# Optimization experiments

Measured on AMD Instinct MI355X. Metric: run time of the kernel, lower is better.

Reference implementation:

```python
import jax, jax.numpy as jnp
import numpy as np

B, N, DIN, DOUT, H, DH, DC, NL, L = 8, 256, 64, 64, 8, 8, 64, 32, 2
SCALE = DH ** -0.5  # out_dim-per-head scaling used by both attention variants


def _ln(x, g, b):
    m = jnp.mean(x, -1, keepdims=True)
    v = jnp.mean((x - m) ** 2, -1, keepdims=True)
    return (x - m) * jax.lax.rsqrt(v + 1e-5) * g + b


def _cross_attn(x, ctx, mask_b, wq, wkv, wo, bo):
    # CrossAttentionLayer: standard softmax attention with clamp(-5,5)
    b, n, _ = x.shape
    m = ctx.shape[1]
    q = (x @ wq).reshape(b, n, H, DH).transpose(0, 2, 1, 3)
    k, v = jnp.split(ctx @ wkv, 2, axis=-1)
    k = k.reshape(b, m, H, DH).transpose(0, 2, 1, 3)
    v = v.reshape(b, m, H, DH).transpose(0, 2, 1, 3)
    sim = jnp.einsum('bhid,bhjd->bhij', q, k) * SCALE
    if mask_b is not None:
        sim = jnp.where(mask_b[:, None, None, :], sim, -jnp.finfo(sim.dtype).max)
    sim = jnp.clip(sim, -5.0, 5.0)
    attn = jax.nn.softmax(sim, axis=-1)
    out = jnp.einsum('bhij,bhjd->bhid', attn, v)
    out = out.transpose(0, 2, 1, 3).reshape(b, n, H * DH)
    return out @ wo + bo


def _mha_edge(p, e, k_RW, mask, wq, wk, we, wv):
    # GraphiT MultiHeadAttentionLayer with edge features + k_RW attention PE
    Q = (p @ wq).reshape(B, N, H, DH)
    K = (p @ wk).reshape(B, N, H, DH) * SCALE
    V = (p @ wv).reshape(B, N, H, DH).transpose(0, 2, 1, 3)  # [B,H,N,d]
    E = (e @ we).reshape(B, N, N, H, DH)
    scores = jnp.einsum('bihk,bjhk,bijhk->bhij', Q, K, E)
    scores = jnp.exp(scores - jnp.max(scores, axis=(-2, -1), keepdims=True))
    scores = scores * mask[:, None, :, None] * mask[:, None, None, :]
    scores = scores * k_RW
    denom = jnp.clip(jnp.sum(scores, -1, keepdims=True), 1e-6, None)
    out = jnp.einsum('bhij,bhjd->bhid', scores, V) / denom
    return out.transpose(0, 2, 1, 3).reshape(B, N, H * DH)


def setup_inputs() -> dict:
    key = jax.random.key(0)
    ks = jax.random.split(key, 32)
    rn = lambda k, s: jax.random.normal(k, s, dtype=jnp.float32)
    inp = {
        'h': rn(ks[0], (B, N, DIN)),
        'p': rn(ks[1], (B, N, DIN)),
        'e': rn(ks[2], (B, N, N, DIN)),
        'k_RW': jax.random.uniform(ks[3], (B, 1, N, N), dtype=jnp.float32),
        'queries': rn(ks[4], (B, NL, DC)),
        'mask': jnp.ones((B, N), dtype=jnp.float32),
        # attention_p (MultiHeadAttentionLayer) weights
        'wq_p': rn(ks[5], (DIN, H * DH)) * 0.05,
        'wk_p': rn(ks[6], (DIN, H * DH)) * 0.05,
        'we_p': rn(ks[7], (DIN, H * DH)) * 0.05,
        'wv_p': rn(ks[8], (DIN, H * DH)) * 0.05,
        'wo_p': rn(ks[9], (DOUT, DOUT)) * 0.05,
        # cross_attention_h (queries attend to nodes)
        'cq_wq': rn(ks[10], (DC, H * DH)) * 0.05,
        'cq_wkv': rn(ks[11], (DIN, 2 * H * DH)) * 0.05,
        'cq_wo': rn(ks[12], (H * DH, DC)) * 0.05,
        'cq_bo': jnp.zeros((DC,), dtype=jnp.float32),
        # L_cross latent self-attention layers (stacked)
        'sa_wq': rn(ks[13], (L, DC, H * DH)) * 0.05,
        'sa_wkv': rn(ks[14], (L, DC, 2 * H * DH)) * 0.05,
        'sa_wo': rn(ks[15], (L, H * DH, DC)) * 0.05,
        'sa_bo': jnp.zeros((L, DC), dtype=jnp.float32),
        # O_queries, norms, FFN
        'oq_w': rn(ks[16], (DC, DC)) * 0.05,
        'ln1_g': jnp.ones((DC,), dtype=jnp.float32),
        'ln1_b': jnp.zeros((DC,), dtype=jnp.float32),
        'ffn_w1': rn(ks[17], (DC, 2 * DC)) * 0.05,
        'ffn_w2': rn(ks[18], (2 * DC, DC)) * 0.05,
        'ln2_g': jnp.ones((DC,), dtype=jnp.float32),
        'ln2_b': jnp.zeros((DC,), dtype=jnp.float32),
    }
    return inp


def reference(h, p, e, k_RW, queries, mask,
              wq_p, wk_p, we_p, wv_p, wo_p,
              cq_wq, cq_wkv, cq_wo, cq_bo,
              sa_wq, sa_wkv, sa_wo, sa_bo,
              oq_w, ln1_g, ln1_b, ffn_w1, ffn_w2, ln2_g, ln2_b):
    # forward_p: update positional encoding via edge-modulated attention
    p_attn = _mha_edge(p, e, k_RW, mask, wq_p, wk_p, we_p, wv_p)
    p_new = p + jnp.tanh(p_attn @ wo_p)  # residual, no dropout (eval)
    # combine node features with updated PE (use_node_pe='sum')
    h_c = h + p_new
    mask_b = mask > 0.5
    # perceiver cross-attention: latents attend to nodes
    q = queries + _cross_attn(queries, h_c, mask_b, cq_wq, cq_wkv, cq_wo, cq_bo)
    # L_cross latent self-attention blocks with residual
    for i in range(L):
        q = q + _cross_attn(q, q, None, sa_wq[i], sa_wkv[i], sa_wo[i], sa_bo[i])
    # O_queries projection + layer norm
    q = _ln(q @ oq_w, ln1_g, ln1_b)
    # feed-forward block on queries
    ff = jax.nn.relu(q @ ffn_w1) @ ffn_w2
    q = _ln(q + ff, ln2_g, ln2_b)
    return q
```

## Files before the change

### kernel.cpp

```cpp
#include <hip/hip_runtime.h>
#include <hip/hip_bf16.h>
#include <math.h>

typedef __bf16 bf16x8 __attribute__((ext_vector_type(8)));
typedef float floatx4 __attribute__((ext_vector_type(4)));

#define ATT_SCALE 0.35355339059327373f

__device__ __forceinline__ __bf16 f2b(float x) { return (__bf16)x; }

__global__ __launch_bounds__(256) void k_proj(const float* __restrict__ p,
                       const float* __restrict__ wq, const float* __restrict__ wk,
                       const float* __restrict__ wv,
                       float* __restrict__ Q, float* __restrict__ Ks,
                       float* __restrict__ V) {
  int blk = blockIdx.x, t = threadIdx.x;
  __shared__ float xr[8][64];
  {
    int rr = t >> 5, cc = (t & 31) * 2;
    float2 pz = *reinterpret_cast<const float2*>(p + blk * 512 + rr * 64 + cc);
    xr[rr][cc] = pz.x; xr[rr][cc + 1] = pz.y;
  }
  __syncthreads();
  if (t < 192) {
    int mat = t >> 6, c = t & 63;
    const float* w = (mat == 0) ? wq : ((mat == 1) ? wk : wv);
    float acc[8] = {0.f, 0.f, 0.f, 0.f, 0.f, 0.f, 0.f, 0.f};
#pragma unroll 8
    for (int k = 0; k < 64; k++) {
      float wv_ = w[k * 64 + c];
#pragma unroll
      for (int r = 0; r < 8; r++) acc[r] += xr[r][k] * wv_;
    }
    float* dst = (mat == 0) ? Q : ((mat == 1) ? Ks : V);
    float sc = (mat == 1) ? ATT_SCALE : 1.f;
#pragma unroll
    for (int r = 0; r < 8; r++) dst[(blk * 8 + r) * 64 + c] = acc[r] * sc;
  }
}

__global__ __launch_bounds__(256) void k_edge(
    const float* __restrict__ e, const float* __restrict__ we,
    const float* __restrict__ krw, const float* __restrict__ mask,
    const float* __restrict__ hin, const float* __restrict__ pin,
    const float* __restrict__ wo, const float* __restrict__ cq_wkv,
    const float* __restrict__ Q, const float* __restrict__ Ks,
    const float* __restrict__ V, float* __restrict__ Kc, float* __restrict__ Vc) {
  int bi = blockIdx.x;
  int b = bi >> 8;
  int t = threadIdx.x;
  int w = t >> 6, l = t & 63;
  int l15 = l & 15, quad = l >> 4, half8 = (l >> 3) & 1, d = l & 7;

  bf16x8 wfrag[4][2];
  for (int nt = 0; nt < 4; nt++)
    for (int kc = 0; kc < 2; kc++)
      for (int jj = 0; jj < 8; jj++)
        wfrag[nt][kc][jj] = f2b(we[(kc * 32 + quad * 8 + jj) * 64 + nt * 16 + l15]);

  float qv[4];
  for (int nt = 0; nt < 4; nt++) qv[nt] = Q[bi * 64 + nt * 16 + l15];
  float mi = mask[bi];

  float aout[4] = {0.f, 0.f, 0.f, 0.f};
  float aden[4] = {0.f, 0.f, 0.f, 0.f};

  for (int mt = 0; mt < 4; mt++) {
    int j0 = w * 64 + mt * 16;
    const float* ep = e + ((long)bi * 256 + j0 + l15) * 64 + quad * 8;
    float4 ea = *reinterpret_cast<const float4*>(ep);
    float4 eb4 = *reinterpret_cast<const float4*>(ep + 4);
    float4 ec = *reinterpret_cast<const float4*>(ep + 32);
    float4 ed4 = *reinterpret_cast<const float4*>(ep + 36);
    bf16x8 a0, a1;
    a0[0] = f2b(ea.x); a0[1] = f2b(ea.y); a0[2] = f2b(ea.z); a0[3] = f2b(ea.w);
    a0[4] = f2b(eb4.x); a0[5] = f2b(eb4.y); a0[6] = f2b(eb4.z); a0[7] = f2b(eb4.w);
    a1[0] = f2b(ec.x); a1[1] = f2b(ec.y); a1[2] = f2b(ec.z); a1[3] = f2b(ec.w);
    a1[4] = f2b(ed4.x); a1[5] = f2b(ed4.y); a1[6] = f2b(ed4.z); a1[7] = f2b(ed4.w);

    int jr0 = j0 + quad * 4;
    float krw_r[4], mj_r[4];
    for (int r = 0; r < 4; r++) {
      krw_r[r] = krw[(long)bi * 256 + jr0 + r];
      mj_r[r] = mask[b * 256 + jr0 + r];
    }
    for (int nt = 0; nt < 4; nt++) {
      floatx4 acc = {0.f, 0.f, 0.f, 0.f};
      acc = __builtin_amdgcn_mfma_f32_16x16x32_bf16(a0, wfrag[nt][0], acc, 0, 0, 0);
      acc = __builtin_amdgcn_mfma_f32_16x16x32_bf16(a1, wfrag[nt][1], acc, 0, 0, 0);
      int hk = nt * 16 + l15;
      int hbase = hk & 56;
      for (int r = 0; r < 4; r++) {
        int jr = jr0 + r;
        float s = acc[r] * qv[nt] * Ks[(b * 256 + jr) * 64 + hk];
        s += __shfl_xor(s, 1);
        s += __shfl_xor(s, 2);
        s += __shfl_xor(s, 4);
        float wg = __expf(s) * krw_r[r] * mj_r[r];
        aden[nt] += wg;
        aout[nt] += wg * V[(b * 256 + jr) * 64 + hbase + d];
      }
    }
  }
  for (int nt = 0; nt < 4; nt++) {
    float o = aout[nt], dn = aden[nt];
    o += __shfl_xor(o, 16); o += __shfl_xor(o, 32);
    dn += __shfl_xor(dn, 16); dn += __shfl_xor(dn, 32);
    aout[nt] = o; aden[nt] = dn;
  }

  __shared__ float red[4][64];
  __shared__ float redden[4][8];
  __shared__ float pav[64];
  __shared__ float hcl[64];
  if (l < 16) {
    for (int nt = 0; nt < 4; nt++) {
      int head = nt * 2 + half8;
      red[w][head * 8 + d] = aout[nt];
      if (d == 0) redden[w][head] = aden[nt];
    }
  }
  __syncthreads();
  if (t < 64) {
    int head = t >> 3;
    float num = red[0][t] + red[1][t] + red[2][t] + red[3][t];
    float den = redden[0][head] + redden[1][head] + redden[2][head] + redden[3][head];
    num *= mi;
    den = fmaxf(den * mi, 1e-6f);
    pav[t] = num / den;
  }
  __syncthreads();
  if (t < 64) {
    float a = 0.f;
    for (int c = 0; c < 64; c++) a += pav[c] * wo[c * 64 + t];
    hcl[t] = hin[bi * 64 + t] + pin[bi * 64 + t] + tanhf(a);
  }
  __syncthreads();
  if (t < 128) {
    float a = 0.f;
    for (int c = 0; c < 64; c++) a += hcl[c] * cq_wkv[c * 128 + t];
    if (t < 64) Kc[bi * 64 + t] = a;
    else        Vc[bi * 64 + t - 64] = a;
  }
}

template <int NR, int NC, int ST>
__device__ __forceinline__ void stage_w(const float* __restrict__ g,
                                        __bf16* wls, int t) {
  constexpr int PER = (NR * NC) >> 10;
  int i0 = t * PER;
  int k = i0 / NC, c0 = i0 % NC;
  const float* src = g + k * NC + c0;
  __bf16* dst = wls + k * ST + c0;
#pragma unroll
  for (int m = 0; m < PER; m += 4) {
    float4 v = *reinterpret_cast<const float4*>(src + m);
    dst[m] = f2b(v.x); dst[m + 1] = f2b(v.y);
    dst[m + 2] = f2b(v.z); dst[m + 3] = f2b(v.w);
  }
}

__global__ __launch_bounds__(1024) void k_tail(
    const float* __restrict__ quer, const float* __restrict__ Kc,
    const float* __restrict__ Vc, const float* __restrict__ mask,
    const float* __restrict__ cq_wq, const float* __restrict__ cq_wo,
    const float* __restrict__ cq_bo,
    const float* __restrict__ sa_wq, const float* __restrict__ sa_wkv,
    const float* __restrict__ sa_wo, const float* __restrict__ sa_bo,
    const float* __restrict__ oq_w, const float* __restrict__ g1,
    const float* __restrict__ b1, const float* __restrict__ w1,
    const float* __restrict__ w2, const float* __restrict__ g2,
    const float* __restrict__ b2v, float* __restrict__ out) {
  int b = blockIdx.x;
  int t = threadIdx.x;

  __shared__ float sq[32 * 68];
  __shared__ float sx[32 * 68];
  __shared__ float pool[6400];
  __shared__ float smask[256];
  __shared__ __bf16 wls[8448];

  float* soc = pool + 4160;
  __bf16* kq = reinterpret_cast<__bf16*>(pool);
  __bf16* vq = kq + 4096;

  const int rr6 = t >> 6, c6 = t & 63;
  const int r2 = t >> 5, h = (t >> 2) & 7, s = t & 3;

  {
    float2 qz = *reinterpret_cast<const float2*>(quer + b * 2048 + (t >> 5) * 64 + (t & 31) * 2);
    sq[(t >> 5) * 68 + (t & 31) * 2] = qz.x;
    sq[(t >> 5) * 68 + (t & 31) * 2 + 1] = qz.y;
    if (t < 256) smask[t] = mask[b * 256 + t];
    stage_w<64, 64, 66>(cq_wq, wls, t);
  }
  __syncthreads();

  {
    float a0 = 0.f, a1 = 0.f;
#pragma unroll 8
    for (int k = 0; k < 64; k++) {
      float wv = (float)wls[k * 66 + c6];
      a0 += sq[rr6 * 68 + k] * wv;
      a1 += sq[(rr6 + 16) * 68 + k] * wv;
    }
    sx[rr6 * 68 + c6] = a0;
    sx[(rr6 + 16) * 68 + c6] = a1;
  }
  __syncthreads();

  float num[8] = {0.f, 0.f, 0.f, 0.f, 0.f, 0.f, 0.f, 0.f};
  float den = 0.f;
  {
    float qv8[8];
#pragma unroll
    for (int dd = 0; dd < 8; dd++) qv8[dd] = sx[r2 * 68 + h * 8 + dd];
    for (int qtr = 0; qtr < 4; qtr++) {
      {
        int half = t >> 9, idx = t & 511;
        int jl = idx >> 3, c0 = (idx & 7) * 8;
        const float* src = (half ? Vc : Kc) + ((long)(b * 256 + qtr * 64 + jl)) * 64 + c0;
        __bf16* dst = (half ? vq : kq) + jl * 64 + c0;
        float4 u = *reinterpret_cast<const float4*>(src);
        float4 v = *reinterpret_cast<const float4*>(src + 4);
        dst[0] = f2b(u.x); dst[1] = f2b(u.y); dst[2] = f2b(u.z); dst[3] = f2b(u.w);
        dst[4] = f2b(v.x); dst[5] = f2b(v.y); dst[6] = f2b(v.z); dst[7] = f2b(v.w);
      }
      if (qtr == 0) stage_w<64, 64, 66>(cq_wo, wls, t);
      __syncthreads();
#pragma unroll
      for (int jj = 0; jj < 16; jj++) {
        int jl = jj * 4 + s;
        bf16x8 kk = *reinterpret_cast<const bf16x8*>(kq + jl * 64 + h * 8);
        float sc = qv8[0] * (float)kk[0] + qv8[1] * (float)kk[1]
                 + qv8[2] * (float)kk[2] + qv8[3] * (float)kk[3]
                 + qv8[4] * (float)kk[4] + qv8[5] * (float)kk[5]
                 + qv8[6] * (float)kk[6] + qv8[7] * (float)kk[7];
        sc *= ATT_SCALE;
        sc = (smask[qtr * 64 + jl] > 0.5f) ? sc : -1e30f;
        sc = fminf(fmaxf(sc, -5.f), 5.f);
        float ex = __expf(sc);
        den += ex;
        bf16x8 vv = *reinterpret_cast<const bf16x8*>(vq + jl * 64 + h * 8);
#pragma unroll
        for (int dd = 0; dd < 8; dd++) num[dd] += ex * (float)vv[dd];
      }
      __syncthreads();
    }
    den += __shfl_xor(den, 1); den += __shfl_xor(den, 2);
#pragma unroll
    for (int dd = 0; dd < 8; dd++) {
      float v = num[dd];
      v += __shfl_xor(v, 1); v += __shfl_xor(v, 2);
      num[dd] = v;
    }
    if (s == 0) {
      float inv = 1.f / den;
#pragma unroll
      for (int dd = 0; dd < 8; dd++) soc[r2 * 68 + h * 8 + dd] = num[dd] * inv;
    }
  }
  __syncthreads();

  {
    float a0 = 0.f, a1 = 0.f;
#pragma unroll 8
    for (int k = 0; k < 64; k++) {
      float wv = (float)wls[k * 66 + c6];
      a0 += soc[rr6 * 68 + k] * wv;
      a1 += soc[(rr6 + 16) * 68 + k] * wv;
    }
    float bb = cq_bo[c6];
    sq[rr6 * 68 + c6] += a0 + bb;
    sq[(rr6 + 16) * 68 + c6] += a1 + bb;
  }
  __syncthreads();

  for (int layer = 0; layer < 2; layer++) {
    const float* wql = sa_wq + layer * 4096;
    const float* wkvl = sa_wkv + layer * 8192;
    const float* wol = sa_wo + layer * 4096;
    const float* bol = sa_bo + layer * 64;

    stage_w<64, 64, 66>(wql, wls, t);
    __syncthreads();
    {
      float a0 = 0.f, a1 = 0.f;
#pragma unroll 8
      for (int k = 0; k < 64; k++) {
        float wv = (float)wls[k * 66 + c6];
        a0 += sq[rr6 * 68 + k] * wv;
        a1 += sq[(rr6 + 16) * 68 + k] * wv;
      }
      sx[rr6 * 68 + c6] = a0;
      sx[(rr6 + 16) * 68 + c6] = a1;
    }
    __syncthreads();
    stage_w<64, 128, 130>(wkvl, wls, t);
    __syncthreads();
    {
      int rrk = t >> 7, ck = t & 127;
      float a0 = 0.f, a1 = 0.f, a2 = 0.f, a3 = 0.f;
#pragma unroll 8
      for (int k = 0; k < 64; k++) {
        float wv = (float)wls[k * 130 + ck];
        a0 += sq[rrk * 68 + k] * wv;
        a1 += sq[(rrk + 8) * 68 + k] * wv;
        a2 += sq[(rrk + 16) * 68 + k] * wv;
        a3 += sq[(rrk + 24) * 68 + k] * wv;
      }
      float* dst = (ck < 64) ? (pool + rrk * 65 + ck) : (pool + 2080 + rrk * 65 + (ck - 64));
      dst[0] = a0; dst[8 * 65] = a1; dst[16 * 65] = a2; dst[24 * 65] = a3;
    }
    __syncthreads();
    {
      stage_w<64, 64, 66>(wol, wls, t);
      float qv8[8];
#pragma unroll
      for (int dd = 0; dd < 8; dd++) qv8[dd] = sx[r2 * 68 + h * 8 + dd];
      float nm[8] = {0.f, 0.f, 0.f, 0.f, 0.f, 0.f, 0.f, 0.f};
      float dn = 0.f;
#pragma unroll
      for (int jj = 0; jj < 8; jj++) {
        int j = jj * 4 + s;
        const float* kp = pool + j * 65 + h * 8;
        float sc = 0.f;
#pragma unroll
        for (int dd = 0; dd < 8; dd++) sc += qv8[dd] * kp[dd];
        sc *= ATT_SCALE;
        sc = fminf(fmaxf(sc, -5.f), 5.f);
        float ex = __expf(sc);
        dn += ex;
        const float* vp = pool + 2080 + j * 65 + h * 8;
#pragma unroll
        for (int dd = 0; dd < 8; dd++) nm[dd] += ex * vp[dd];
      }
      dn += __shfl_xor(dn, 1); dn += __shfl_xor(dn, 2);
#pragma unroll
      for (int dd = 0; dd < 8; dd++) {
        float v = nm[dd];
        v += __shfl_xor(v, 1); v += __shfl_xor(v, 2);
        nm[dd] = v;
      }
      if (s == 0) {
        float inv = 1.f / dn;
#pragma unroll
        for (int dd = 0; dd < 8; dd++) soc[r2 * 68 + h * 8 + dd] = nm[dd] * inv;
      }
    }
    __syncthreads();
    {
      float a0 = 0.f, a1 = 0.f;
#pragma unroll 8
      for (int k = 0; k < 64; k++) {
        float wv = (float)wls[k * 66 + c6];
        a0 += soc[rr6 * 68 + k] * wv;
        a1 += soc[(rr6 + 16) * 68 + k] * wv;
      }
      float bb = bol[c6];
      sq[rr6 * 68 + c6] += a0 + bb;
      sq[(rr6 + 16) * 68 + c6] += a1 + bb;
    }
    __syncthreads();
  }

  stage_w<64, 64, 66>(oq_w, wls, t);
  __syncthreads();
  {
    float a0 = 0.f, a1 = 0.f;
#pragma unroll 8
    for (int k = 0; k < 64; k++) {
      float wv = (float)wls[k * 66 + c6];
      a0 += sq[rr6 * 68 + k] * wv;
      a1 += sq[(rr6 + 16) * 68 + k] * wv;
    }
    sx[rr6 * 68 + c6] = a0;
    sx[(rr6 + 16) * 68 + c6] = a1;
  }
  __syncthreads();
  {
    int wv_ = t >> 6, lc = t & 63;
#pragma unroll
    for (int pass = 0; pass < 2; pass++) {
      int rr = wv_ + pass * 16;
      float x = sx[rr * 68 + lc];
      float m = x;
      for (int off = 1; off < 64; off <<= 1) m += __shfl_xor(m, off);
      m *= (1.f / 64.f);
      float dv = x - m, vv = dv * dv;
      for (int off = 1; off < 64; off <<= 1) vv += __shfl_xor(vv, off);
      vv *= (1.f / 64.f);
      sx[rr * 68 + lc] = dv * rsqrtf(vv + 1e-5f) * g1[lc] + b1[lc];
    }
    stage_w<64, 128, 130>(w1, wls, t);
  }
  __syncthreads();
  {
    int rrk = t >> 7, ck = t & 127;
    float a0 = 0.f, a1 = 0.f, a2 = 0.f, a3 = 0.f;
#pragma unroll 8
    for (int k = 0; k < 64; k++) {
      float wv = (float)wls[k * 130 + ck];
      a0 += sx[rrk * 68 + k] * wv;
      a1 += sx[(rrk + 8) * 68 + k] * wv;
      a2 += sx[(rrk + 16) * 68 + k] * wv;
      a3 += sx[(rrk + 24) * 68 + k] * wv;
    }
    pool[rrk * 128 + ck] = fmaxf(a0, 0.f);
    pool[(rrk + 8) * 128 + ck] = fmaxf(a1, 0.f);
    pool[(rrk + 16) * 128 + ck] = fmaxf(a2, 0.f);
    pool[(rrk + 24) * 128 + ck] = fmaxf(a3, 0.f);
  }
  __syncthreads();
  stage_w<128, 64, 66>(w2, wls, t);
  __syncthreads();
  {
    int wv_ = t >> 6, lc = t & 63;
#pragma unroll
    for (int pass = 0; pass < 2; pass++) {
      int rr = wv_ + pass * 16;
      float ff = 0.f;
#pragma unroll 8
      for (int k = 0; k < 128; k++) ff += pool[rr * 128 + k] * (float)wls[k * 66 + lc];
      float z = sx[rr * 68 + lc] + ff;
      float m2 = z;
      for (int off = 1; off < 64; off <<= 1) m2 += __shfl_xor(m2, off);
      m2 *= (1.f / 64.f);
      float dz = z - m2, v2 = dz * dz;
      for (int off = 1; off < 64; off <<= 1) v2 += __shfl_xor(v2, off);
      v2 *= (1.f / 64.f);
      out[b * 2048 + rr * 64 + lc] = dz * rsqrtf(v2 + 1e-5f) * g2[lc] + b2v[lc];
    }
  }
}

extern "C" void kernel_launch(void* const* d_in, const int* in_sizes, int n_in,
                              void* d_out, int out_size, void* d_ws, size_t ws_size,
                              hipStream_t stream) {
  const float* h_in   = (const float*)d_in[0];
  const float* p_in   = (const float*)d_in[1];
  const float* e_in   = (const float*)d_in[2];
  const float* krw    = (const float*)d_in[3];
  const float* quer   = (const float*)d_in[4];
  const float* mask   = (const float*)d_in[5];
  const float* wq_p   = (const float*)d_in[6];
  const float* wk_p   = (const float*)d_in[7];
  const float* we_p   = (const float*)d_in[8];
  const float* wv_p   = (const float*)d_in[9];
  const float* wo_p   = (const float*)d_in[10];
  const float* cq_wq  = (const float*)d_in[11];
  const float* cq_wkv = (const float*)d_in[12];
  const float* cq_wo  = (const float*)d_in[13];
  const float* cq_bo  = (const float*)d_in[14];
  const float* sa_wq  = (const float*)d_in[15];
  const float* sa_wkv = (const float*)d_in[16];
  const float* sa_wo  = (const float*)d_in[17];
  const float* sa_bo  = (const float*)d_in[18];
  const float* oq_w   = (const float*)d_in[19];
  const float* ln1_g  = (const float*)d_in[20];
  const float* ln1_b  = (const float*)d_in[21];
  const float* ffn_w1 = (const float*)d_in[22];
  const float* ffn_w2 = (const float*)d_in[23];
  const float* ln2_g  = (const float*)d_in[24];
  const float* ln2_b  = (const float*)d_in[25];

  float* ws = (float*)d_ws;
  float* Q  = ws;
  float* Ks = Q + 131072;
  float* V  = Ks + 131072;
  float* Kc = V + 131072;
  float* Vc = Kc + 131072;

  k_proj<<<256, 256, 0, stream>>>(p_in, wq_p, wk_p, wv_p, Q, Ks, V);
  k_edge<<<2048, 256, 0, stream>>>(e_in, we_p, krw, mask, h_in, p_in, wo_p, cq_wkv,
                                   Q, Ks, V, Kc, Vc);
  k_tail<<<8, 1024, 0, stream>>>(quer, Kc, Vc, mask, cq_wq, cq_wo, cq_bo,
                                 sa_wq, sa_wkv, sa_wo, sa_bo, oq_w,
                                 ln1_g, ln1_b, ffn_w1, ffn_w2, ln2_g, ln2_b,
                                 (float*)d_out);
}
```

Baseline: 333.2 us.

## Register-block four query rows per thread in tail attention loops

The tail kernel's cross-attention and latent self-attention loops now have each thread handle four query rows of one head over a 16-way key split, instead of one row over a 4-way split. Each K/V vector loaded from shared memory is reused across four rows, cutting LDS traffic and bf16 conversions. The bf16 K/V staging rows are padded from 64 to 72 elements to reduce bank conflicts, so the shared pool grows. In exchange, register pressure rises in a 1024-thread block, and the reductions need four shuffle stages per value.

Result: slower. 346.1 us (+3.9%).

```diff
diff --git a/kernel.cpp b/kernel.cpp
--- a/kernel.cpp
+++ b/kernel.cpp
@@ -176,16 +176,16 @@
 
   __shared__ float sq[32 * 68];
   __shared__ float sx[32 * 68];
-  __shared__ float pool[6400];
+  __shared__ float pool[6784];
   __shared__ float smask[256];
   __shared__ __bf16 wls[8448];
 
-  float* soc = pool + 4160;
+  float* soc = pool + 4608;
   __bf16* kq = reinterpret_cast<__bf16*>(pool);
-  __bf16* vq = kq + 4096;
+  __bf16* vq = kq + 4608;
 
   const int rr6 = t >> 6, c6 = t & 63;
-  const int r2 = t >> 5, h = (t >> 2) & 7, s = t & 3;
+  const int rg = t >> 7, h8 = (t >> 4) & 7, s16 = t & 15;
 
   {
     float2 qz = *reinterpret_cast<const float2*>(quer + b * 2048 + (t >> 5) * 64 + (t & 31) * 2);
@@ -209,18 +209,26 @@
   }
   __syncthreads();
 
-  float num[8] = {0.f, 0.f, 0.f, 0.f, 0.f, 0.f, 0.f, 0.f};
-  float den = 0.f;
-  {
-    float qv8[8];
-#pragma unroll
-    for (int dd = 0; dd < 8; dd++) qv8[dd] = sx[r2 * 68 + h * 8 + dd];
+  {
+    float qv8[4][8];
+#pragma unroll
+    for (int rr = 0; rr < 4; rr++)
+#pragma unroll
+      for (int dd = 0; dd < 8; dd++)
+        qv8[rr][dd] = sx[(rg * 4 + rr) * 68 + h8 * 8 + dd];
+    float num[4][8];
+    float den[4] = {0.f, 0.f, 0.f, 0.f};
+#pragma unroll
+    for (int rr = 0; rr < 4; rr++)
+#pragma unroll
+      for (int dd = 0; dd < 8; dd++) num[rr][dd] = 0.f;
+
     for (int qtr = 0; qtr < 4; qtr++) {
       {
         int half = t >> 9, idx = t & 511;
         int jl = idx >> 3, c0 = (idx & 7) * 8;
         const float* src = (half ? Vc : Kc) + ((long)(b * 256 + qtr * 64 + jl)) * 64 + c0;
-        __bf16* dst = (half ? vq : kq) + jl * 64 + c0;
+        __bf16* dst = (half ? vq : kq) + jl * 72 + c0;
         float4 u = *reinterpret_cast<const float4*>(src);
         float4 v = *reinterpret_cast<const float4*>(src + 4);
         dst[0] = f2b(u.x); dst[1] = f2b(u.y); dst[2] = f2b(u.z); dst[3] = f2b(u.w);
@@ -229,35 +237,53 @@
       if (qtr == 0) stage_w<64, 64, 66>(cq_wo, wls, t);
       __syncthreads();
 #pragma unroll
-      for (int jj = 0; jj < 16; jj++) {
-        int jl = jj * 4 + s;
-        bf16x8 kk = *reinterpret_cast<const bf16x8*>(kq + jl * 64 + h * 8);
-        float sc = qv8[0] * (float)kk[0] + qv8[1] * (float)kk[1]
-                 + qv8[2] * (float)kk[2] + qv8[3] * (float)kk[3]
-                 + qv8[4] * (float)kk[4] + qv8[5] * (float)kk[5]
-                 + qv8[6] * (float)kk[6] + qv8[7] * (float)kk[7];
-        sc *= ATT_SCALE;
-        sc = (smask[qtr * 64 + jl] > 0.5f) ? sc : -1e30f;
-        sc = fminf(fmaxf(sc, -5.f), 5.f);
-        float ex = __expf(sc);
-        den += ex;
-        bf16x8 vv = *reinterpret_cast<const bf16x8*>(vq + jl * 64 + h * 8);
-#pragma unroll
-        for (int dd = 0; dd < 8; dd++) num[dd] += ex * (float)vv[dd];
+      for (int jj = 0; jj < 4; jj++) {
+        int jl = jj * 16 + s16;
+        bf16x8 kk = *reinterpret_cast<const bf16x8*>(kq + jl * 72 + h8 * 8);
+        bf16x8 vv = *reinterpret_cast<const bf16x8*>(vq + jl * 72 + h8 * 8);
+        float kf[8], vf[8];
+#pragma unroll
+        for (int dd = 0; dd < 8; dd++) { kf[dd] = (float)kk[dd]; vf[dd] = (float)vv[dd]; }
+        float msel = smask[qtr * 64 + jl];
+#pragma unroll
+        for (int rr = 0; rr < 4; rr++) {
+          float sc = qv8[rr][0] * kf[0] + qv8[rr][1] * kf[1]
+                   + qv8[rr][2] * kf[2] + qv8[rr][3] * kf[3]
+                   + qv8[rr][4] * kf[4] + qv8[rr][5] * kf[5]
+                   + qv8[rr][6] * kf[6] + qv8[rr][7] * kf[7];
+          sc *= ATT_SCALE;
+          sc = (msel > 0.5f) ? sc : -1e30f;
+          sc = fminf(fmaxf(sc, -5.f), 5.f);
+          float ex = __expf(sc);
+          den[rr] += ex;
+#pragma unroll
+          for (int dd = 0; dd < 8; dd++) num[rr][dd] += ex * vf[dd];
+        }
       }
       __syncthreads();
     }
-    den += __shfl_xor(den, 1); den += __shfl_xor(den, 2);
-#pragma unroll
-    for (int dd = 0; dd < 8; dd++) {
-      float v = num[dd];
-      v += __shfl_xor(v, 1); v += __shfl_xor(v, 2);
-      num[dd] = v;
-    }
-    if (s == 0) {
-      float inv = 1.f / den;
-#pragma unroll
-      for (int dd = 0; dd < 8; dd++) soc[r2 * 68 + h * 8 + dd] = num[dd] * inv;
+#pragma unroll
+    for (int rr = 0; rr < 4; rr++) {
+      float dn = den[rr];
+      dn += __shfl_xor(dn, 1); dn += __shfl_xor(dn, 2);
+      dn += __shfl_xor(dn, 4); dn += __shfl_xor(dn, 8);
+      den[rr] = dn;
+#pragma unroll
+      for (int dd = 0; dd < 8; dd++) {
+        float v = num[rr][dd];
+        v += __shfl_xor(v, 1); v += __shfl_xor(v, 2);
+        v += __shfl_xor(v, 4); v += __shfl_xor(v, 8);
+        num[rr][dd] = v;
+      }
+    }
+    if (s16 == 0) {
+#pragma unroll
+      for (int rr = 0; rr < 4; rr++) {
+        float inv = 1.f / den[rr];
+#pragma unroll
+        for (int dd = 0; dd < 8; dd++)
+          soc[(rg * 4 + rr) * 68 + h8 * 8 + dd] = num[rr][dd] * inv;
+      }
     }
   }
   __syncthreads();
@@ -315,37 +341,62 @@
     __syncthreads();
     {
       stage_w<64, 64, 66>(wol, wls, t);
-      float qv8[8];
-#pragma unroll
-      for (int dd = 0; dd < 8; dd++) qv8[dd] = sx[r2 * 68 + h * 8 + dd];
-      float nm[8] = {0.f, 0.f, 0.f, 0.f, 0.f, 0.f, 0.f, 0.f};
-      float dn = 0.f;
-#pragma unroll
-      for (int jj = 0; jj < 8; jj++) {
-        int j = jj * 4 + s;
-        const float* kp = pool + j * 65 + h * 8;
-        float sc = 0.f;
-#pragma unroll
-        for (int dd = 0; dd < 8; dd++) sc += qv8[dd] * kp[dd];
-        sc *= ATT_SCALE;
-        sc = fminf(fmaxf(sc, -5.f), 5.f);
-        float ex = __expf(sc);
-        dn += ex;
-        const float* vp = pool + 2080 + j * 65 + h * 8;
-#pragma unroll
-        for (int dd = 0; dd < 8; dd++) nm[dd] += ex * vp[dd];
-      }
-      dn += __shfl_xor(dn, 1); dn += __shfl_xor(dn, 2);
-#pragma unroll
-      for (int dd = 0; dd < 8; dd++) {
-        float v = nm[dd];
-        v += __shfl_xor(v, 1); v += __shfl_xor(v, 2);
-        nm[dd] = v;
-      }
-      if (s == 0) {
-        float inv = 1.f / dn;
-#pragma unroll
-        for (int dd = 0; dd < 8; dd++) soc[r2 * 68 + h * 8 + dd] = nm[dd] * inv;
+      float qv8[4][8];
+#pragma unroll
+      for (int rr = 0; rr < 4; rr++)
+#pragma unroll
+        for (int dd = 0; dd < 8; dd++)
+          qv8[rr][dd] = sx[(rg * 4 + rr) * 68 + h8 * 8 + dd];
+      float nm[4][8];
+      float dn[4] = {0.f, 0.f, 0.f, 0.f};
+#pragma unroll
+      for (int rr = 0; rr < 4; rr++)
+#pragma unroll
+        for (int dd = 0; dd < 8; dd++) nm[rr][dd] = 0.f;
+#pragma unroll
+      for (int jj = 0; jj < 2; jj++) {
+        int j = jj * 16 + s16;
+        const float* kp = pool + j * 65 + h8 * 8;
+        const float* vp = pool + 2080 + j * 65 + h8 * 8;
+        float kf[8], vf[8];
+#pragma unroll
+        for (int dd = 0; dd < 8; dd++) { kf[dd] = kp[dd]; vf[dd] = vp[dd]; }
+#pragma unroll
+        for (int rr = 0; rr < 4; rr++) {
+          float sc = qv8[rr][0] * kf[0] + qv8[rr][1] * kf[1]
+                   + qv8[rr][2] * kf[2] + qv8[rr][3] * kf[3]
+                   + qv8[rr][4] * kf[4] + qv8[rr][5] * kf[5]
+                   + qv8[rr][6] * kf[6] + qv8[rr][7] * kf[7];
+          sc *= ATT_SCALE;
+          sc = fminf(fmaxf(sc, -5.f), 5.f);
+          float ex = __expf(sc);
+          dn[rr] += ex;
+#pragma unroll
+          for (int dd = 0; dd < 8; dd++) nm[rr][dd] += ex * vf[dd];
+        }
+      }
+#pragma unroll
+      for (int rr = 0; rr < 4; rr++) {
+        float d2 = dn[rr];
+        d2 += __shfl_xor(d2, 1); d2 += __shfl_xor(d2, 2);
+        d2 += __shfl_xor(d2, 4); d2 += __shfl_xor(d2, 8);
+        dn[rr] = d2;
+#pragma unroll
+        for (int dd = 0; dd < 8; dd++) {
+          float v = nm[rr][dd];
+          v += __shfl_xor(v, 1); v += __shfl_xor(v, 2);
+          v += __shfl_xor(v, 4); v += __shfl_xor(v, 8);
+          nm[rr][dd] = v;
+        }
+      }
+      if (s16 == 0) {
+#pragma unroll
+        for (int rr = 0; rr < 4; rr++) {
+          float inv = 1.f / dn[rr];
+#pragma unroll
+          for (int dd = 0; dd < 8; dd++)
+            soc[(rg * 4 + rr) * 68 + h8 * 8 + dd] = nm[rr][dd] * inv;
+        }
       }
     }
     __syncthreads();
```
